# Optimization experiments

Measured on AMD Instinct MI355X. Metric: run time of the kernel, lower is better.

Reference implementation:

```python
import jax, jax.numpy as jnp
import numpy as np
import math

SEQ = 2048
D_MODEL = 1024
HEADS = 16
D_K = D_MODEL // HEADS
B = 2


def setup_inputs() -> dict:
    key = jax.random.key(0)
    k1, k2, k3, k4, k5 = jax.random.split(key, 5)
    s = 1.0 / math.sqrt(D_MODEL)
    x = jax.random.normal(k1, (B, SEQ, D_MODEL), dtype=jnp.float32)
    w_qkv = jax.random.normal(k2, (D_MODEL, 3 * D_MODEL), dtype=jnp.float32) * s
    b_qkv = jax.random.normal(k3, (3 * D_MODEL,), dtype=jnp.float32) * 0.01
    w_out = jax.random.normal(k4, (D_MODEL, D_MODEL), dtype=jnp.float32) * s
    b_out = jax.random.normal(k5, (D_MODEL,), dtype=jnp.float32) * 0.01
    return {"x": x, "w_qkv": w_qkv, "b_qkv": b_qkv, "w_out": w_out, "b_out": b_out}


def _rope_tables():
    inv_freq = 1.0 / (10000.0 ** (jnp.arange(0, D_K, 2, dtype=jnp.float32) / D_K))
    angles = jnp.arange(SEQ, dtype=jnp.float32)[:, None] * inv_freq[None, :]  # [S, d_k/2]
    return jnp.sin(angles), jnp.cos(angles)


def _apply_rope(x, sin, cos):
    # x: [H, B, S, d_k]; interleaved pairing: x1 = even lanes, x2 = odd lanes
    xp = x.reshape(*x.shape[:-1], D_K // 2, 2)
    x1, x2 = xp[..., 0], xp[..., 1]
    r1 = x1 * cos - x2 * sin
    r2 = x1 * sin + x2 * cos
    return jnp.stack([r1, r2], axis=-1).reshape(x.shape)


def reference(x, w_qkv, b_qkv, w_out, b_out):
    qkv = x @ w_qkv + b_qkv                     # [B, S, 3D]
    q, k, v = jnp.split(qkv, 3, axis=-1)        # each [B, S, D]

    def to_heads(t):  # chunk last dim into heads -> [H, B, S, d_k]
        return t.reshape(B, SEQ, HEADS, D_K).transpose(2, 0, 1, 3)

    q, k, v = to_heads(q), to_heads(k), to_heads(v)
    sin, cos = _rope_tables()
    q = _apply_rope(q, sin, cos)
    k = _apply_rope(k, sin, cos)

    # NOTE: original divides by scale = 1/sqrt(d_k) -> multiply by sqrt(d_k)
    scores = jnp.einsum('hbqd,hbkd->hbqk', q, k) * math.sqrt(D_K)
    causal = jnp.tril(jnp.ones((SEQ, SEQ), dtype=bool))
    scores = jnp.where(causal, scores, -jnp.inf)
    attn = jax.nn.softmax(scores, axis=-1)      # dropout_prob = 0.0
    out = jnp.einsum('hbqk,hbkd->hbqd', attn, v)  # [H, B, S, d_k]
    concat = out.transpose(1, 2, 0, 3).reshape(B, SEQ, D_MODEL)
    return concat @ w_out + b_out
```

## Files before the change

kernel.cpp:

```cpp
#include <hip/hip_runtime.h>


typedef __attribute__((ext_vector_type(8))) short s16x8;
typedef __attribute__((ext_vector_type(8))) unsigned short u16x8;
typedef __attribute__((ext_vector_type(4))) float f32x4;
typedef __attribute__((ext_vector_type(4))) int i32x4;

#define L2E 1.44269504088896340736f

__device__ __forceinline__ unsigned short f2bf(float f) {
  unsigned int u = __builtin_bit_cast(unsigned int, f);
  u += 0x7FFFu + ((u >> 16) & 1u);
  return (unsigned short)(u >> 16);
}
__device__ __forceinline__ float bf2f(unsigned short h) {
  unsigned int u = ((unsigned int)h) << 16;
  return __builtin_bit_cast(float, u);
}

__device__ __forceinline__ void gload16(const void* g, void* l) {
  __builtin_amdgcn_global_load_lds(
      (const __attribute__((address_space(1))) unsigned int*)g,
      (__attribute__((address_space(3))) unsigned int*)l, 16, 0, 0);
}

__global__ __launch_bounds__(256) void split_x_kernel(
    const float* __restrict__ x, unsigned short* __restrict__ xhi,
    unsigned short* __restrict__ xlo) {
  size_t i = ((size_t)blockIdx.x * 256 + threadIdx.x) * 8;
  f32x4 a = *(const f32x4*)(x + i);
  f32x4 c = *(const f32x4*)(x + i + 4);
  u16x8 h, lo;
#pragma unroll
  for (int j = 0; j < 4; ++j) {
    unsigned short hv = f2bf(a[j]);
    h[j] = hv; lo[j] = f2bf(a[j] - bf2f(hv));
    unsigned short hv2 = f2bf(c[j]);
    h[4 + j] = hv2; lo[4 + j] = f2bf(c[j] - bf2f(hv2));
  }
  *(u16x8*)(xhi + i) = h;
  *(u16x8*)(xlo + i) = lo;
}

__global__ __launch_bounds__(256) void transpose_split_kernel(
    const float* __restrict__ W, unsigned short* __restrict__ Thi,
    unsigned short* __restrict__ Tlo, int N, int hasLo) {
  __shared__ unsigned short hi[64][72];
  __shared__ unsigned short lo[64][72];
  const int t = threadIdx.x;
  const int k0 = blockIdx.x * 64, n0 = blockIdx.y * 64;
#pragma unroll
  for (int r = 0; r < 16; ++r) {
    int kk = r * 4 + (t >> 6);
    int nn = t & 63;
    float v = W[(size_t)(k0 + kk) * N + n0 + nn];
    unsigned short hv = f2bf(v);
    hi[nn][kk] = hv;
    lo[nn][kk] = f2bf(v - bf2f(hv));
  }
  __syncthreads();
#pragma unroll
  for (int i = 0; i < 2; ++i) {
    int ci = t + i * 256;
    int nn = ci >> 3, kc = (ci & 7) * 8;
    u16x8 vh, vl;
#pragma unroll
    for (int j = 0; j < 8; ++j) { vh[j] = hi[nn][kc + j]; vl[j] = lo[nn][kc + j]; }
    *(u16x8*)(Thi + (size_t)(n0 + nn) * 1024 + k0 + kc) = vh;
    if (hasLo) *(u16x8*)(Tlo + (size_t)(n0 + nn) * 1024 + k0 + kc) = vl;
  }
}

__global__ __launch_bounds__(256) void rope_tab_kernel(float* __restrict__ tab) {
  int idx = blockIdx.x * 256 + threadIdx.x;
  int s = idx >> 5, i = idx & 31;
  float invf = exp2f(-(float)i * 0.4152410118609203f);
  float ang = (float)s * invf;
  tab[idx] = cosf(ang);
  tab[65536 + idx] = sinf(ang);
}

__global__ __launch_bounds__(256) void gemm_qkv_kernel(
    const unsigned short* __restrict__ xhi, const unsigned short* __restrict__ xlo,
    const unsigned short* __restrict__ whi, const unsigned short* __restrict__ wlo,
    const float* __restrict__ bqkv, const float* __restrict__ ctab,
    unsigned short* __restrict__ Qsb, unsigned short* __restrict__ Ksb,
    unsigned short* __restrict__ vbufT) {
  __shared__ alignas(16) unsigned short sh[32768];
  const int tid = threadIdx.x, w = tid >> 6, l = tid & 63;
  const int l15 = l & 15, l4 = l >> 4;
  const int m0 = blockIdx.x * 128, n0 = blockIdx.y * 128;
  const int wrow = w >> 1, wcol = w & 1;
  const int which = n0 >> 10;
  const bool isV = (which == 2);
  const float* stab = ctab + 65536;
  const int g_row = l >> 2;
  const int g_col = (l & 3) * 8;

  f32x4 acc[4][4] = {};

#define STAGEP(p_) do {                                                        \
    int kk_ = (p_) * 32;                                                       \
    unsigned short* lb0_ = sh + (((p_) & 1) << 14) + (w * 2) * 512;            \
    _Pragma("unroll")                                                          \
    for (int i = 0; i < 2; ++i) {                                              \
      int rb_ = (w * 2 + i) * 16 + g_row;                                      \
      unsigned short* lb_ = lb0_ + i * 512;                                    \
      gload16(xhi + (size_t)(m0 + rb_) * 1024 + kk_ + g_col, lb_);             \
      gload16(whi + (size_t)(n0 + rb_) * 1024 + kk_ + g_col, lb_ + 4096);      \
      if (!isV) {                                                              \
        gload16(wlo + (size_t)(n0 + rb_) * 1024 + kk_ + g_col, lb_ + 8192);    \
        gload16(xlo + (size_t)(m0 + rb_) * 1024 + kk_ + g_col, lb_ + 12288);   \
      }                                                                        \
    }                                                                          \
  } while (0)

  STAGEP(0);
  __syncthreads();
  for (int p = 0; p < 32; ++p) {
    if (p + 1 < 32) STAGEP(p + 1);
    const unsigned short* bp = sh + ((p & 1) << 14);
    s16x8 af[4], bfr[4];
#pragma unroll
    for (int g = 0; g < 4; ++g) {
      af[g] = *(const s16x8*)(bp + (wrow * 64 + g * 16 + l15) * 32 + l4 * 8);
      bfr[g] = *(const s16x8*)(bp + 4096 + (wcol * 64 + g * 16 + l15) * 32 + l4 * 8);
    }
#pragma unroll
    for (int rg = 0; rg < 4; ++rg)
#pragma unroll
      for (int cg = 0; cg < 4; ++cg)
        acc[rg][cg] = __builtin_amdgcn_mfma_f32_16x16x32_bf16(af[rg], bfr[cg], acc[rg][cg], 0, 0, 0);
    if (!isV) {
      s16x8 bl[4], al[4];
#pragma unroll
      for (int g = 0; g < 4; ++g) {
        bl[g] = *(const s16x8*)(bp + 8192 + (wcol * 64 + g * 16 + l15) * 32 + l4 * 8);
        al[g] = *(const s16x8*)(bp + 12288 + (wrow * 64 + g * 16 + l15) * 32 + l4 * 8);
      }
#pragma unroll
      for (int rg = 0; rg < 4; ++rg)
#pragma unroll
        for (int cg = 0; cg < 4; ++cg)
          acc[rg][cg] = __builtin_amdgcn_mfma_f32_16x16x32_bf16(af[rg], bl[cg], acc[rg][cg], 0, 0, 0);
#pragma unroll
      for (int rg = 0; rg < 4; ++rg)
#pragma unroll
        for (int cg = 0; cg < 4; ++cg)
          acc[rg][cg] = __builtin_amdgcn_mfma_f32_16x16x32_bf16(al[rg], bfr[cg], acc[rg][cg], 0, 0, 0);
    }
    __syncthreads();
  }
#undef STAGEP

  const int n_head0 = (n0 & 1023) >> 6;
  const int bb = m0 >> 11;
  const int s_base = m0 & 2047;
  unsigned short* stg = sh;

  if (isV) {
#pragma unroll
    for (int cg = 0; cg < 4; ++cg) {
      int n_local = wcol * 64 + cg * 16 + l15;
      float bias = bqkv[n0 + n_local];
      int swz = (n_local & 7) << 3;
#pragma unroll
      for (int rg = 0; rg < 4; ++rg)
#pragma unroll
        for (int r = 0; r < 4; ++r) {
          int m_local = wrow * 64 + rg * 16 + l4 * 4 + r;
          stg[n_local * 128 + (m_local ^ swz)] = f2bf(acc[rg][cg][r] + bias);
        }
    }
    __syncthreads();
#pragma unroll
    for (int i = 0; i < 8; ++i) {
      int c = i * 256 + tid;
      int n = c >> 4, piece = c & 15;
      int hh = n_head0 + (n >> 6), d = n & 63;
      unsigned short* dst =
          vbufT + ((size_t)(bb * 16 + hh)) * 131072 + d * 2048 + s_base + piece * 8;
      *(i32x4*)dst = *(const i32x4*)(stg + n * 128 + ((piece * 8) ^ ((n & 7) << 3)));
    }
  } else {
    unsigned short* qk = which ? Ksb : Qsb;
    const float sc8 = which ? 1.0f : 8.0f;
#pragma unroll
    for (int cg = 0; cg < 4; ++cg) {
      int n_local = wcol * 64 + cg * 16 + l15;
      int dk = n_local & 63;
      int ih = dk >> 1;
      float bias = bqkv[n0 + n_local];
#pragma unroll
      for (int rg = 0; rg < 4; ++rg)
#pragma unroll
        for (int r = 0; r < 4; ++r) {
          int s = s_base + wrow * 64 + rg * 16 + l4 * 4 + r;
          float v = acc[rg][cg][r] + bias;
          float p = __shfl_xor(v, 1);
          float cs = ctab[(s << 5) + ih];
          float sn = stab[(s << 5) + ih];
          float rr = (dk & 1) ? (p * sn + v * cs) : (v * cs - p * sn);
          acc[rg][cg][r] = rr * sc8;
        }
    }
#pragma unroll
    for (int pass = 0; pass < 2; ++pass) {
#pragma unroll
      for (int cg = 0; cg < 4; ++cg) {
        int n_local = wcol * 64 + cg * 16 + l15;
#pragma unroll
        for (int rg = 0; rg < 4; ++rg)
#pragma unroll
          for (int r = 0; r < 4; ++r) {
            int m_local = wrow * 64 + rg * 16 + l4 * 4 + r;
            float rr = acc[rg][cg][r];
            unsigned short hv = f2bf(rr);
            stg[m_local * 128 + n_local] = pass ? f2bf(rr - bf2f(hv)) : hv;
          }
      }
      __syncthreads();
#pragma unroll
      for (int i = 0; i < 8; ++i) {
        int c = i * 256 + tid;
        int hh_l = c >> 10, row = (c >> 3) & 127, piece = c & 7;
        int hh = n_head0 + hh_l;
        unsigned short* dst =
            qk + (((size_t)bb * 16 + hh) * 2048 + s_base + row) * 128 + pass * 64;
        *(i32x4*)(dst + piece * 8) = *(const i32x4*)(stg + row * 128 + hh_l * 64 + piece * 8);
      }
      __syncthreads();
    }
  }
}

__global__ __launch_bounds__(512, 4) void flash_kernel(
    const unsigned short* __restrict__ Qs, const unsigned short* __restrict__ Ks,
    const unsigned short* __restrict__ VbT, unsigned short* __restrict__ attn) {
  __shared__ alignas(16) unsigned short Khi[2][64 * 64];
  __shared__ alignas(16) unsigned short Klo[2][64 * 64];
  __shared__ alignas(16) unsigned short Vt[2][64 * 64];
  __shared__ alignas(16) unsigned short Pl[8][16 * 64];

  const int tid = threadIdx.x;
  const int wv = tid >> 6, l = tid & 63;
  const int l15 = l & 15, l4 = l >> 4;

  const int sid = blockIdx.x;
  const int idx = (sid & 255) >> 5;
  const int strip = (sid >> 8) ? idx : 15 - idx;
  const int hb = sid & 31;
  const int h = hb & 15, b = hb >> 4;
  const int qb = strip * 128;

  const size_t bh = (size_t)(b * 16 + h);
  const unsigned short* Qbase = Qs + bh * 2048 * 128;
  const unsigned short* Kbase = Ks + bh * 2048 * 128;
  const unsigned short* Vbase = VbT + bh * 131072;

  s16x8 qf[2][2];
  {
    int q = qb + wv * 16 + l15;
    const unsigned short* qr = Qbase + (size_t)q * 128;
#pragma unroll
    for (int ks = 0; ks < 2; ++ks) {
      qf[0][ks] = *(const s16x8*)(qr + ks * 32 + l4 * 8);
      qf[1][ks] = *(const s16x8*)(qr + 64 + ks * 32 + l4 * 8);
    }
  }

  f32x4 acc[4] = {};
  float mrow[4], lrow[4];
#pragma unroll
  for (int r = 0; r < 4; ++r) { mrow[r] = -1e38f; lrow[r] = 0.f; }

  const int row = tid >> 3;
  const int cb = (tid & 7) * 16;

  i32x4 kh, kl, vv;
#define PREF(kt_) do {                                                        \
    int kv0_ = (kt_) * 64;                                                    \
    const char* s_ = (const char*)(Kbase + (size_t)(kv0_ + row) * 128);       \
    kh = *(const i32x4*)(s_ + cb);  kl = *(const i32x4*)(s_ + 128 + cb);      \
    vv = *(const i32x4*)((const char*)(Vbase + (size_t)row * 2048 + kv0_) + cb); \
  } while (0)

#define STAGE(bf_) do {                                                       \
    int sw = cb ^ ((row & 7) << 4);                                           \
    *(i32x4*)((char*)Khi[bf_] + row * 128 + sw) = kh;                         \
    *(i32x4*)((char*)Klo[bf_] + row * 128 + sw) = kl;                         \
    *(i32x4*)((char*)Vt[bf_] + row * 128 + sw) = vv;                          \
  } while (0)

  const int nt = (qb >> 6) + 2;
  PREF(0);
  STAGE(0);
  if (nt > 1) PREF(1);
  __syncthreads();

  for (int kt = 0; kt < nt; ++kt) {
    const int kv0 = kt * 64;
    const int cur = kt & 1;
    if (kt + 1 < nt) {
      STAGE(cur ^ 1);
      if (kt + 2 < nt) PREF(kt + 2);
    }

    f32x4 sc[4];
#pragma unroll
    for (int cg = 0; cg < 4; ++cg) {
      int kr = cg * 16 + l15;
      int swz = (kr & 7) << 4;
      const char* ph = (const char*)Khi[cur] + kr * 128;
      const char* pl2 = (const char*)Klo[cur] + kr * 128;
      s16x8 kbh[2], kbl[2];
#pragma unroll
      for (int ks = 0; ks < 2; ++ks) {
        int off = (ks * 64 + l4 * 16) ^ swz;
        kbh[ks] = *(const s16x8*)(ph + off);
        kbl[ks] = *(const s16x8*)(pl2 + off);
      }
      __builtin_amdgcn_s_setprio(1);
      f32x4 a = {0.f, 0.f, 0.f, 0.f};
#pragma unroll
      for (int ks = 0; ks < 2; ++ks) {
        a = __builtin_amdgcn_mfma_f32_16x16x32_bf16(qf[0][ks], kbh[ks], a, 0, 0, 0);
        a = __builtin_amdgcn_mfma_f32_16x16x32_bf16(qf[0][ks], kbl[ks], a, 0, 0, 0);
        a = __builtin_amdgcn_mfma_f32_16x16x32_bf16(qf[1][ks], kbh[ks], a, 0, 0, 0);
      }
      __builtin_amdgcn_s_setprio(0);
      sc[cg] = a;
    }

    if (kt >= (qb >> 6)) {
#pragma unroll
      for (int cg = 0; cg < 4; ++cg)
#pragma unroll
        for (int r = 0; r < 4; ++r) {
          int q = qb + wv * 16 + l4 * 4 + r;
          int kv = kv0 + cg * 16 + l15;
          if (kv > q) sc[cg][r] = -1e38f;
        }
    }

    {
      float vmax[4];
      bool cnd = true;
#pragma unroll
      for (int r = 0; r < 4; ++r) {
        float v = fmaxf(fmaxf(sc[0][r], sc[1][r]), fmaxf(sc[2][r], sc[3][r]));
        v = fmaxf(v, __shfl_xor(v, 1));
        v = fmaxf(v, __shfl_xor(v, 2));
        v = fmaxf(v, __shfl_xor(v, 4));
        v = fmaxf(v, __shfl_xor(v, 8));
        vmax[r] = v;
        cnd = cnd && (v <= mrow[r] + 8.0f);
      }
      const bool defer = __all(cnd ? 1 : 0);
      float al[4];
      if (!defer) {
#pragma unroll
        for (int r = 0; r < 4; ++r) {
          float mn = fmaxf(mrow[r], vmax[r]);
          al[r] = exp2f((mrow[r] - mn) * L2E);
          mrow[r] = mn;
        }
      }
      float rs[4];
#pragma unroll
      for (int r = 0; r < 4; ++r) rs[r] = 0.f;
#pragma unroll
      for (int cg = 0; cg < 4; ++cg)
#pragma unroll
        for (int r = 0; r < 4; ++r) {
          float p = exp2f((sc[cg][r] - mrow[r]) * L2E);
          sc[cg][r] = p;
          rs[r] += p;
        }
#pragma unroll
      for (int r = 0; r < 4; ++r) {
        float v = rs[r];
        v += __shfl_xor(v, 1);
        v += __shfl_xor(v, 2);
        v += __shfl_xor(v, 4);
        v += __shfl_xor(v, 8);
        rs[r] = v;
      }
      if (defer) {
#pragma unroll
        for (int r = 0; r < 4; ++r) lrow[r] += rs[r];
      } else {
#pragma unroll
        for (int r = 0; r < 4; ++r) lrow[r] = lrow[r] * al[r] + rs[r];
#pragma unroll
        for (int dg = 0; dg < 4; ++dg)
#pragma unroll
          for (int r = 0; r < 4; ++r) acc[dg][r] *= al[r];
      }
#pragma unroll
      for (int cg = 0; cg < 4; ++cg)
#pragma unroll
        for (int r = 0; r < 4; ++r) {
          int roww = l4 * 4 + r;
          int colb = (cg * 16 + l15) * 2;
          int addr = roww * 128 + (colb ^ ((roww & 7) << 4));
          *(unsigned short*)((char*)Pl[wv] + addr) = f2bf(sc[cg][r]);
        }
    }

    {
      s16x8 pf[2];
      int swz = (l15 & 7) << 4;
#pragma unroll
      for (int kc = 0; kc < 2; ++kc)
        pf[kc] = *(const s16x8*)((const char*)Pl[wv] + l15 * 128 + ((kc * 64 + l4 * 16) ^ swz));
      __builtin_amdgcn_s_setprio(1);
#pragma unroll
      for (int dg = 0; dg < 4; ++dg) {
        int dr = dg * 16 + l15;
        int swzd = (dr & 7) << 4;
#pragma unroll
        for (int kc = 0; kc < 2; ++kc) {
          s16x8 vf = *(const s16x8*)((const char*)Vt[cur] + dr * 128 + ((kc * 64 + l4 * 16) ^ swzd));
          acc[dg] = __builtin_amdgcn_mfma_f32_16x16x32_bf16(pf[kc], vf, acc[dg], 0, 0, 0);
        }
      }
      __builtin_amdgcn_s_setprio(0);
    }
    __syncthreads();
  }
#undef PREF
#undef STAGE

  {
    unsigned short* stg = (unsigned short*)Pl;
#pragma unroll
    for (int r = 0; r < 4; ++r) {
      float inv = 1.0f / lrow[r];
      int row_local = wv * 16 + l4 * 4 + r;
#pragma unroll
      for (int dg = 0; dg < 4; ++dg)
        stg[row_local * 64 + dg * 16 + l15] = f2bf(acc[dg][r] * inv);
    }
    __syncthreads();
#pragma unroll
    for (int i = 0; i < 2; ++i) {
      int c = i * 512 + tid;
      int rw = c >> 3, piece = c & 7;
      unsigned short* dst = attn + ((size_t)(b * 2048 + qb + rw)) * 1024 + h * 64;
      *(i32x4*)(dst + piece * 8) = *(const i32x4*)(stg + rw * 64 + piece * 8);
    }
  }
}

__global__ __launch_bounds__(256) void gemm_out_kernel(
    const unsigned short* __restrict__ attn, const unsigned short* __restrict__ wot,
    const float* __restrict__ bout, float* __restrict__ out) {
  __shared__ alignas(16) unsigned short As[128 * 64];
  __shared__ alignas(16) unsigned short Bs[128 * 64];
  const int tid = threadIdx.x, w = tid >> 6, l = tid & 63;
  const int l15 = l & 15, l4 = l >> 4;
  const int m0 = blockIdx.x * 128, n0 = blockIdx.y * 128;
  const int wrow = w >> 1, wcol = w & 1;
  const int crow = w * 32 + (l >> 3);
  const int lcol8 = (l & 7) * 8;

  f32x4 acc[4][4] = {};
  u16x8 ra0, ra1, ra2, ra3, rb0, rb1, rb2, rb3;

#define LOADT(kt_) do {                                                       \
    int k0_ = (kt_) * 64;                                                     \
    const unsigned short* ap_ = attn + (size_t)(m0 + crow) * 1024 + k0_ + lcol8; \
    const unsigned short* bp_ = wot + (size_t)(n0 + crow) * 1024 + k0_ + lcol8;  \
    ra0 = *(const u16x8*)(ap_);         rb0 = *(const u16x8*)(bp_);           \
    ra1 = *(const u16x8*)(ap_ + 8192);  rb1 = *(const u16x8*)(bp_ + 8192);    \
    ra2 = *(const u16x8*)(ap_ + 16384); rb2 = *(const u16x8*)(bp_ + 16384);   \
    ra3 = *(const u16x8*)(ap_ + 24576); rb3 = *(const u16x8*)(bp_ + 24576);   \
  } while (0)

  LOADT(0);
  for (int kt = 0; kt < 16; ++kt) {
    __syncthreads();
    {
      int base = w * 2048 + l * 8;
      *(u16x8*)(As + base)        = ra0;  *(u16x8*)(Bs + base)        = rb0;
      *(u16x8*)(As + base + 512)  = ra1;  *(u16x8*)(Bs + base + 512)  = rb1;
      *(u16x8*)(As + base + 1024) = ra2;  *(u16x8*)(Bs + base + 1024) = rb2;
      *(u16x8*)(As + base + 1536) = ra3;  *(u16x8*)(Bs + base + 1536) = rb3;
    }
    __syncthreads();
    if (kt < 15) LOADT(kt + 1);
#pragma unroll
    for (int ks = 0; ks < 2; ++ks) {
      s16x8 af[4], bfr[4];
#pragma unroll
      for (int g = 0; g < 4; ++g) {
        af[g] = *(const s16x8*)(As + (wrow * 64 + g * 16 + l15) * 64 + ks * 32 + l4 * 8);
        bfr[g] = *(const s16x8*)(Bs + (wcol * 64 + g * 16 + l15) * 64 + ks * 32 + l4 * 8);
      }
#pragma unroll
      for (int rg = 0; rg < 4; ++rg)
#pragma unroll
        for (int cg = 0; cg < 4; ++cg)
          acc[rg][cg] = __builtin_amdgcn_mfma_f32_16x16x32_bf16(af[rg], bfr[cg], acc[rg][cg], 0, 0, 0);
    }
  }
#undef LOADT

#pragma unroll
  for (int cg = 0; cg < 4; ++cg) {
    int n = n0 + wcol * 64 + cg * 16 + l15;
    float bias = bout[n];
#pragma unroll
    for (int rg = 0; rg < 4; ++rg) {
#pragma unroll
      for (int r = 0; r < 4; ++r) {
        int m = m0 + wrow * 64 + rg * 16 + l4 * 4 + r;
        out[(size_t)m * 1024 + n] = acc[rg][cg][r] + bias;
      }
    }
  }
}

#define OFF_XHI 0ull
#define OFF_ATT 0ull
#define OFF_XLO 8388608ull
#define OFF_WHI 16777216ull
#define OFF_WLO 23068672ull
#define OFF_WOT 29360128ull
#define OFF_QS  31457280ull
#define OFF_KS  48234496ull
#define OFF_V   65011712ull

extern "C" void kernel_launch(void* const* d_in, const int* in_sizes, int n_in,
                              void* d_out, int out_size, void* d_ws, size_t ws_size,
                              hipStream_t stream) {
  (void)in_sizes; (void)n_in; (void)out_size; (void)ws_size;
  const float* x     = (const float*)d_in[0];
  const float* w_qkv = (const float*)d_in[1];
  const float* b_qkv = (const float*)d_in[2];
  const float* w_out = (const float*)d_in[3];
  const float* b_out = (const float*)d_in[4];
  float* out = (float*)d_out;
  char* ws = (char*)d_ws;

  unsigned short* xhi = (unsigned short*)(ws + OFF_XHI);
  unsigned short* xlo = (unsigned short*)(ws + OFF_XLO);
  unsigned short* whi = (unsigned short*)(ws + OFF_WHI);
  unsigned short* wlo = (unsigned short*)(ws + OFF_WLO);
  unsigned short* wot = (unsigned short*)(ws + OFF_WOT);
  unsigned short* Qsb = (unsigned short*)(ws + OFF_QS);
  unsigned short* Ksb = (unsigned short*)(ws + OFF_KS);
  unsigned short* vbT = (unsigned short*)(ws + OFF_V);
  unsigned short* att = (unsigned short*)(ws + OFF_ATT);

  float* rtab = out;

  split_x_kernel<<<2048, 256, 0, stream>>>(x, xhi, xlo);
  transpose_split_kernel<<<dim3(16, 48), 256, 0, stream>>>(w_qkv, whi, wlo, 3072, 1);
  transpose_split_kernel<<<dim3(16, 16), 256, 0, stream>>>(w_out, wot, nullptr, 1024, 0);
  rope_tab_kernel<<<256, 256, 0, stream>>>(rtab);
  gemm_qkv_kernel<<<dim3(32, 24), 256, 0, stream>>>(xhi, xlo, whi, wlo, b_qkv, rtab, Qsb, Ksb, vbT);
  flash_kernel<<<512, 512, 0, stream>>>(Qsb, Ksb, vbT, att);
  gemm_out_kernel<<<dim3(32, 8), 256, 0, stream>>>(att, wot, b_out, out);
}
```

Before: 202.4 us.

## Compute softmax row sums via MFMA and use async LDS loads in out-proj GEMM

In the attention kernel, the per-row softmax denominator is now accumulated by an extra MFMA of the probability fragment against a vector of bf16 ones, replacing the shuffle-based row-sum reduction and separate lrow bookkeeping. In the output projection GEMM, register-staged global loads are replaced by direct global-to-LDS loads into a double buffer with a K step of 32, using one barrier per step. This removes shuffle and VALU work from the softmax and cuts register staging and barriers in the GEMM, at the cost of extra MFMA issue and a denominator built from bf16-rounded probabilities.

```diff
diff --git a/kernel.cpp b/kernel.cpp
--- a/kernel.cpp
+++ b/kernel.cpp
@@ -269,10 +269,15 @@
     }
   }
 
+  s16x8 vones;
+#pragma unroll
+  for (int j = 0; j < 8; ++j) vones[j] = (short)0x3F80;
+
   f32x4 acc[4] = {};
-  float mrow[4], lrow[4];
-#pragma unroll
-  for (int r = 0; r < 4; ++r) { mrow[r] = -1e38f; lrow[r] = 0.f; }
+  f32x4 accl = {};
+  float mrow[4];
+#pragma unroll
+  for (int r = 0; r < 4; ++r) mrow[r] = -1e38f;
 
   const int row = tid >> 3;
   const int cb = (tid & 7) * 16;
@@ -357,46 +362,22 @@
         cnd = cnd && (v <= mrow[r] + 8.0f);
       }
       const bool defer = __all(cnd ? 1 : 0);
-      float al[4];
       if (!defer) {
 #pragma unroll
         for (int r = 0; r < 4; ++r) {
           float mn = fmaxf(mrow[r], vmax[r]);
-          al[r] = exp2f((mrow[r] - mn) * L2E);
+          float al = exp2f((mrow[r] - mn) * L2E);
           mrow[r] = mn;
+          accl[r] *= al;
+#pragma unroll
+          for (int dg = 0; dg < 4; ++dg) acc[dg][r] *= al;
         }
       }
-      float rs[4];
-#pragma unroll
-      for (int r = 0; r < 4; ++r) rs[r] = 0.f;
 #pragma unroll
       for (int cg = 0; cg < 4; ++cg)
 #pragma unroll
-        for (int r = 0; r < 4; ++r) {
-          float p = exp2f((sc[cg][r] - mrow[r]) * L2E);
-          sc[cg][r] = p;
-          rs[r] += p;
-        }
-#pragma unroll
-      for (int r = 0; r < 4; ++r) {
-        float v = rs[r];
-        v += __shfl_xor(v, 1);
-        v += __shfl_xor(v, 2);
-        v += __shfl_xor(v, 4);
-        v += __shfl_xor(v, 8);
-        rs[r] = v;
-      }
-      if (defer) {
-#pragma unroll
-        for (int r = 0; r < 4; ++r) lrow[r] += rs[r];
-      } else {
-#pragma unroll
-        for (int r = 0; r < 4; ++r) lrow[r] = lrow[r] * al[r] + rs[r];
-#pragma unroll
-        for (int dg = 0; dg < 4; ++dg)
-#pragma unroll
-          for (int r = 0; r < 4; ++r) acc[dg][r] *= al[r];
-      }
+        for (int r = 0; r < 4; ++r)
+          sc[cg][r] = exp2f((sc[cg][r] - mrow[r]) * L2E);
 #pragma unroll
       for (int cg = 0; cg < 4; ++cg)
 #pragma unroll
@@ -425,6 +406,9 @@
           acc[dg] = __builtin_amdgcn_mfma_f32_16x16x32_bf16(pf[kc], vf, acc[dg], 0, 0, 0);
         }
       }
+#pragma unroll
+      for (int kc = 0; kc < 2; ++kc)
+        accl = __builtin_amdgcn_mfma_f32_16x16x32_bf16(pf[kc], vones, accl, 0, 0, 0);
       __builtin_amdgcn_s_setprio(0);
     }
     __syncthreads();
@@ -436,7 +420,7 @@
     unsigned short* stg = (unsigned short*)Pl;
 #pragma unroll
     for (int r = 0; r < 4; ++r) {
-      float inv = 1.0f / lrow[r];
+      float inv = 1.0f / accl[r];
       int row_local = wv * 16 + l4 * 4 + r;
 #pragma unroll
       for (int dg = 0; dg < 4; ++dg)
@@ -456,56 +440,46 @@
 __global__ __launch_bounds__(256) void gemm_out_kernel(
     const unsigned short* __restrict__ attn, const unsigned short* __restrict__ wot,
     const float* __restrict__ bout, float* __restrict__ out) {
-  __shared__ alignas(16) unsigned short As[128 * 64];
-  __shared__ alignas(16) unsigned short Bs[128 * 64];
+  __shared__ alignas(16) unsigned short sh[16384];
   const int tid = threadIdx.x, w = tid >> 6, l = tid & 63;
   const int l15 = l & 15, l4 = l >> 4;
   const int m0 = blockIdx.x * 128, n0 = blockIdx.y * 128;
   const int wrow = w >> 1, wcol = w & 1;
-  const int crow = w * 32 + (l >> 3);
-  const int lcol8 = (l & 7) * 8;
+  const int g_row = l >> 2, g_col = (l & 3) * 8;
 
   f32x4 acc[4][4] = {};
-  u16x8 ra0, ra1, ra2, ra3, rb0, rb1, rb2, rb3;
-
-#define LOADT(kt_) do {                                                       \
-    int k0_ = (kt_) * 64;                                                     \
-    const unsigned short* ap_ = attn + (size_t)(m0 + crow) * 1024 + k0_ + lcol8; \
-    const unsigned short* bp_ = wot + (size_t)(n0 + crow) * 1024 + k0_ + lcol8;  \
-    ra0 = *(const u16x8*)(ap_);         rb0 = *(const u16x8*)(bp_);           \
-    ra1 = *(const u16x8*)(ap_ + 8192);  rb1 = *(const u16x8*)(bp_ + 8192);    \
-    ra2 = *(const u16x8*)(ap_ + 16384); rb2 = *(const u16x8*)(bp_ + 16384);   \
-    ra3 = *(const u16x8*)(ap_ + 24576); rb3 = *(const u16x8*)(bp_ + 24576);   \
+
+#define STAGEP(p_) do {                                                        \
+    int kk_ = (p_) * 32;                                                       \
+    unsigned short* lb0_ = sh + (((p_) & 1) << 13) + (w * 2) * 512;            \
+    _Pragma("unroll")                                                          \
+    for (int i = 0; i < 2; ++i) {                                              \
+      int rb_ = (w * 2 + i) * 16 + g_row;                                      \
+      unsigned short* lb_ = lb0_ + i * 512;                                    \
+      gload16(attn + (size_t)(m0 + rb_) * 1024 + kk_ + g_col, lb_);            \
+      gload16(wot + (size_t)(n0 + rb_) * 1024 + kk_ + g_col, lb_ + 4096);      \
+    }                                                                          \
   } while (0)
 
-  LOADT(0);
-  for (int kt = 0; kt < 16; ++kt) {
+  STAGEP(0);
+  __syncthreads();
+  for (int p = 0; p < 32; ++p) {
+    if (p + 1 < 32) STAGEP(p + 1);
+    const unsigned short* bp = sh + ((p & 1) << 13);
+    s16x8 af[4], bfr[4];
+#pragma unroll
+    for (int g = 0; g < 4; ++g) {
+      af[g] = *(const s16x8*)(bp + (wrow * 64 + g * 16 + l15) * 32 + l4 * 8);
+      bfr[g] = *(const s16x8*)(bp + 4096 + (wcol * 64 + g * 16 + l15) * 32 + l4 * 8);
+    }
+#pragma unroll
+    for (int rg = 0; rg < 4; ++rg)
+#pragma unroll
+      for (int cg = 0; cg < 4; ++cg)
+        acc[rg][cg] = __builtin_amdgcn_mfma_f32_16x16x32_bf16(af[rg], bfr[cg], acc[rg][cg], 0, 0, 0);
     __syncthreads();
-    {
-      int base = w * 2048 + l * 8;
-      *(u16x8*)(As + base)        = ra0;  *(u16x8*)(Bs + base)        = rb0;
-      *(u16x8*)(As + base + 512)  = ra1;  *(u16x8*)(Bs + base + 512)  = rb1;
-      *(u16x8*)(As + base + 1024) = ra2;  *(u16x8*)(Bs + base + 1024) = rb2;
-      *(u16x8*)(As + base + 1536) = ra3;  *(u16x8*)(Bs + base + 1536) = rb3;
-    }
-    __syncthreads();
-    if (kt < 15) LOADT(kt + 1);
-#pragma unroll
-    for (int ks = 0; ks < 2; ++ks) {
-      s16x8 af[4], bfr[4];
-#pragma unroll
-      for (int g = 0; g < 4; ++g) {
-        af[g] = *(const s16x8*)(As + (wrow * 64 + g * 16 + l15) * 64 + ks * 32 + l4 * 8);
-        bfr[g] = *(const s16x8*)(Bs + (wcol * 64 + g * 16 + l15) * 64 + ks * 32 + l4 * 8);
-      }
-#pragma unroll
-      for (int rg = 0; rg < 4; ++rg)
-#pragma unroll
-        for (int cg = 0; cg < 4; ++cg)
-          acc[rg][cg] = __builtin_amdgcn_mfma_f32_16x16x32_bf16(af[rg], bfr[cg], acc[rg][cg], 0, 0, 0);
-    }
-  }
-#undef LOADT
+  }
+#undef STAGEP
 
 #pragma unroll
   for (int cg = 0; cg < 4; ++cg) {
```

New measurement: 192.7 us. -4.8%, faster.
